# Kernel optimization log

Hardware: AMD Instinct MI355X
Metric: run time of the kernel (lower is better)

## Reference

```python
import jax, jax.numpy as jnp
import numpy as np

B, T, C, H = 4, 2048, 1024, 8
D = C // H


def _rope_tables(t, d, base=10000.0):
    inv = 1.0 / (base ** (jnp.arange(0, d, 2, dtype=jnp.float32) / d))
    freqs = jnp.outer(jnp.arange(t, dtype=jnp.float32), inv)  # (T, D/2)
    cos = jnp.concatenate([jnp.cos(freqs)] * 2, axis=-1)  # (T, D)
    sin = jnp.concatenate([jnp.sin(freqs)] * 2, axis=-1)
    return cos, sin


def _apply_rope(x, cos, sin):
    # x: (B,H,T,D); rotate-half RoPE
    d2 = x.shape[-1] // 2
    x1, x2 = x[..., :d2], x[..., d2:]
    rot = jnp.concatenate([-x2, x1], axis=-1)
    return x * cos + rot * sin


def setup_inputs() -> dict:
    key = jax.random.key(0)
    ks = jax.random.split(key, 8)
    x = jax.random.normal(ks[0], (B, T, C), jnp.float32)
    w = lambda k: jax.random.normal(k, (C, C), jnp.float32) * 0.02
    # trigram directions: 8 sign patterns in {-1,+1}^3, L2-normalized (as in get_trigrams + F.normalize)
    signs = np.array([[(1 if (i >> b) & 1 else -1) for b in range(3)] for i in range(8)], np.float32)
    head_dirs = jnp.asarray(signs / np.sqrt(3.0))
    return {
        'x': x,
        'Wq': w(ks[1]), 'Wk': w(ks[2]), 'Wv': w(ks[3]), 'Wo': w(ks[4]),
        'ln_g': jnp.ones((C,), jnp.float32), 'ln_b': jnp.zeros((C,), jnp.float32),
        'head_scales': jax.random.normal(ks[5], (H,), jnp.float32) * 0.1,
        'head_dirs': head_dirs,
    }


def reference(x, Wq, Wk, Wv, Wo, ln_g, ln_b, head_scales, head_dirs):
    b, t, c = x.shape
    h = head_dirs.shape[0]
    d = c // h
    scale = 1.0 / jnp.sqrt(jnp.asarray(d, x.dtype))
    # pre-LN
    mu = jnp.mean(x, axis=-1, keepdims=True)
    var = jnp.mean((x - mu) ** 2, axis=-1, keepdims=True)
    xn = (x - mu) * jax.lax.rsqrt(var + 1e-5) * ln_g + ln_b
    q = (xn @ Wq.T).reshape(b, t, h, d).transpose(0, 2, 1, 3)  # (B,H,T,D)
    k = (xn @ Wk.T).reshape(b, t, h, d).transpose(0, 2, 1, 3)
    v = (xn @ Wv.T).reshape(b, t, h, d).transpose(0, 2, 1, 3)
    cos, sin = _rope_tables(t, d)
    q = _apply_rope(q, cos, sin)
    k = _apply_rope(k, cos, sin)
    causal = jnp.tril(jnp.ones((t, t), bool))
    # standard causal SDPA
    scores = jnp.einsum('bhqd,bhkd->bhqk', q, k) * scale
    scores = jnp.where(causal, scores, -jnp.inf)
    attn = jax.nn.softmax(scores, axis=-1)
    out = jnp.einsum('bhqk,bhkd->bhqd', attn, v)
    # trigram geometric bias attention (rank-1 logits from first 3 dims)
    qp = jnp.einsum('bhtd,hd->bht', q[..., :3], head_dirs)
    kp = jnp.einsum('bhtd,hd->bht', k[..., :3], head_dirs)
    geo = qp[..., :, None] * kp[..., None, :]  # (B,H,T,T)
    geo = jnp.where(causal, geo, -jnp.inf)
    geo_attn = jax.nn.softmax(geo, axis=-1)
    geo_out = jnp.einsum('bhqk,bhkd->bhqd', geo_attn, v)
    out = out + head_scales[None, :, None, None] * jax.lax.stop_gradient(geo_out - out)
    out = out.transpose(0, 2, 1, 3).reshape(b, t, c) @ Wo.T
    return x + out
```

## Files before the change

kernel.cpp:

```cpp
#include <hip/hip_runtime.h>
#include <hip/hip_bf16.h>
#include <stdint.h>

#define BB 4
#define TT 2048
#define CC 1024
#define HH 8
#define DD 128

typedef unsigned short u16;
typedef unsigned int u32;
typedef unsigned long long u64;
typedef __attribute__((ext_vector_type(4))) float f32x4;
typedef __attribute__((ext_vector_type(16))) float f32x16;
typedef __attribute__((ext_vector_type(8))) __bf16 bf16x8;

#define SL2C (0.08838834764831845f * 1.442695040888963f)

__device__ __forceinline__ float bf2f(u16 u){ u32 x=((u32)u)<<16; float f; __builtin_memcpy(&f,&x,4); return f; }
__device__ __forceinline__ u16 f2bf(float f){ u32 x; __builtin_memcpy(&x,&f,4); x += 0x7fffu + ((x>>16)&1u); return (u16)(x>>16); }

__device__ __forceinline__ void gload16(const void* g, void* l){
  __builtin_amdgcn_global_load_lds((const __attribute__((address_space(1))) u32*)g,
                                   (__attribute__((address_space(3))) u32*)l, 16, 0, 0);
}
__device__ __forceinline__ f32x4 mfma16(bf16x8 a, bf16x8 b, f32x4 c){
  return __builtin_amdgcn_mfma_f32_16x16x32_bf16(a,b,c,0,0,0);
}
__device__ __forceinline__ f32x16 mfma32(bf16x8 a, bf16x8 b, f32x16 c){
  return __builtin_amdgcn_mfma_f32_32x32x16_bf16(a,b,c,0,0,0);
}
__device__ __forceinline__ u32 cvtpk(float lo, float hi){
  u32 r; asm("v_cvt_pk_bf16_f32 %0, %1, %2" : "=v"(r) : "v"(lo), "v"(hi)); return r;
}
__device__ __forceinline__ void pl32swap(u32& d, u32& s){
  asm volatile("v_permlane32_swap_b32 %0, %1" : "+v"(d), "+v"(s));
}
union FRAG { u32 u[4]; bf16x8 v; };

__global__ void ln_k(const float* __restrict__ x, const float* __restrict__ g,
                     const float* __restrict__ bta, u16* __restrict__ xn){
  int row = blockIdx.x, tid = threadIdx.x;
  const float4 v = ((const float4*)(x + (size_t)row*CC))[tid];
  float s = v.x+v.y+v.z+v.w;
  float ss = v.x*v.x+v.y*v.y+v.z*v.z+v.w*v.w;
  #pragma unroll
  for(int m=1;m<64;m<<=1){ s += __shfl_xor(s,m); ss += __shfl_xor(ss,m); }
  __shared__ float red[8];
  if((tid&63)==0){ red[tid>>6]=s; red[4+(tid>>6)]=ss; }
  __syncthreads();
  float ts = red[0]+red[1]+red[2]+red[3];
  float tss = red[4]+red[5]+red[6]+red[7];
  float mu = ts*(1.0f/CC);
  float rs = rsqrtf(tss*(1.0f/CC) - mu*mu + 1e-5f);
  int c0 = tid*4;
  ushort4 o;
  o.x = f2bf((v.x-mu)*rs*g[c0+0]+bta[c0+0]);
  o.y = f2bf((v.y-mu)*rs*g[c0+1]+bta[c0+1]);
  o.z = f2bf((v.z-mu)*rs*g[c0+2]+bta[c0+2]);
  o.w = f2bf((v.w-mu)*rs*g[c0+3]+bta[c0+3]);
  ((ushort4*)(xn + (size_t)row*CC))[tid] = o;
}

__global__ void prep_k(const float* __restrict__ wq, const float* __restrict__ wk,
                       const float* __restrict__ wv, const float* __restrict__ wo,
                       u16* __restrict__ out, float* __restrict__ cosT, float* __restrict__ sinT){
  if(blockIdx.x < 4096){
    int i = blockIdx.x*256 + threadIdx.x;
    int sel = i>>18;
    const float* src = sel==0?wq: sel==1?wk: sel==2?wv:wo;
    float4 v = ((const float4*)src)[i & 262143];
    ushort4 o; o.x=f2bf(v.x); o.y=f2bf(v.y); o.z=f2bf(v.z); o.w=f2bf(v.w);
    ((ushort4*)out)[i] = o;
  } else {
    int i = (blockIdx.x-4096)*256 + threadIdx.x;
    int t = i>>6, j = i&63;
    float inv = powf(10000.0f, -(float)(2*j)*(1.0f/128.0f));
    float a = (float)t * inv;
    cosT[i] = cosf(a);
    sinT[i] = sinf(a);
  }
}

__global__ void qpkp_k(const u16* __restrict__ Qb, const u16* __restrict__ KF,
                       const float* __restrict__ dirs, float* __restrict__ qp, float* __restrict__ kp){
  const float INV_SL2 = 1.0f/SL2C;
  int idx = blockIdx.x*256 + threadIdx.x;
  int b = idx>>14, rem = idx & 16383;
  int h = rem>>11, t = rem & 2047;
  int bh = b*HH + h;
  float d0 = dirs[h*3], d1 = dirs[h*3+1], d2 = dirs[h*3+2];
  size_t qbase = ((size_t)(b*TT + t))*CC + h*DD;
  qp[idx] = (bf2f(Qb[qbase])*d0 + bf2f(Qb[qbase+1])*d1 + bf2f(Qb[qbase+2])*d2) * INV_SL2;
  size_t kb = ((size_t)(bh*64 + (t>>5))*8)*512 + (size_t)(t&31)*8;
  kp[idx] = bf2f(KF[kb])*d0 + bf2f(KF[kb+1])*d1 + bf2f(KF[kb+2])*d2;
}

template<int MODE>
__global__ __launch_bounds__(256) void gemm_k(const u16* __restrict__ A, const u16* __restrict__ W,
                                              u16* __restrict__ outb, float* __restrict__ outf,
                                              const float* __restrict__ resid,
                                              const float* __restrict__ cosT, const float* __restrict__ sinT){
  __shared__ __align__(16) u16 sbuf[16384];
  u16* As = sbuf;
  u16* Bs = sbuf + 8192;
  const int K = CC;
  int m0 = blockIdx.x*128, n0 = blockIdx.y*128;
  int tid = threadIdx.x, w = tid>>6, l = tid&63;
  int li = l&15, lg = l>>4;
  int wm = w>>1, wn = w&1;
  f32x4 acc[4][4] = {};
  for(int k0=0; k0<K; k0+=64){
    #pragma unroll
    for(int i=0;i<4;i++){
      int L = (w*4+i)*1024 + l*16;
      int row = L>>7;
      int colb = (L&127) ^ ((row&7)<<4);
      gload16(A + ((size_t)(m0+row)*K + k0 + (colb>>1)), (char*)As + (w*4+i)*1024);
      gload16(W + ((size_t)(n0+row)*K + k0 + (colb>>1)), (char*)Bs + (w*4+i)*1024);
    }
    __syncthreads();
    #pragma unroll
    for(int kc=0;kc<2;kc++){
      bf16x8 af[4], bfr[4];
      #pragma unroll
      for(int mi=0;mi<4;mi++){
        int row = wm*64 + mi*16 + li;
        int colb = (kc*64 + lg*16) ^ ((row&7)<<4);
        af[mi] = *(const bf16x8*)((const char*)As + row*128 + colb);
      }
      #pragma unroll
      for(int ni=0;ni<4;ni++){
        int row = wn*64 + ni*16 + li;
        int colb = (kc*64 + lg*16) ^ ((row&7)<<4);
        bfr[ni] = *(const bf16x8*)((const char*)Bs + row*128 + colb);
      }
      #pragma unroll
      for(int mi=0;mi<4;mi++){
        #pragma unroll
        for(int ni=0;ni<4;ni++)
          acc[mi][ni] = mfma16(af[mi], bfr[ni], acc[mi][ni]);
      }
    }
    __syncthreads();
  }

  if(MODE==0 || MODE==5){
    #pragma unroll
    for(int mi=0;mi<4;mi++){
      #pragma unroll
      for(int ni=0;ni<4;ni++){
        int c = wn*64 + ni*16 + li;
        #pragma unroll
        for(int r=0;r<4;r++){
          int rr = wm*64 + mi*16 + lg*4 + r;
          sbuf[rr*128 + (c ^ ((rr&15)<<3))] = f2bf(acc[mi][ni][r]);
        }
      }
    }
    __syncthreads();
    int rowl = tid & 127, half = tid >> 7;
    int grow = m0 + rowl;
    int t = grow & (TT-1);
    int swz = (rowl&15)<<3;
    const float* cbase = cosT + t*64;
    const float* sbase = sinT + t*64;
    #pragma unroll
    for(int g=0; g<16; g++){
      int c0 = half*64 + g*4;
      int j0 = c0 & 63;
      float4 cv = *(const float4*)(cbase + j0);
      float4 sv4 = *(const float4*)(sbase + j0);
      ushort4 se4 = *(const ushort4*)&sbuf[rowl*128 + (c0 ^ swz)];
      ushort4 pa4 = *(const ushort4*)&sbuf[rowl*128 + ((c0^64) ^ swz)];
      float se[4] = {bf2f(se4.x),bf2f(se4.y),bf2f(se4.z),bf2f(se4.w)};
      float pa[4] = {bf2f(pa4.x),bf2f(pa4.y),bf2f(pa4.z),bf2f(pa4.w)};
      float cc4[4] = {cv.x,cv.y,cv.z,cv.w};
      float ss4[4] = {sv4.x,sv4.y,sv4.z,sv4.w};
      ushort4 o; u16* op = (u16*)&o;
      #pragma unroll
      for(int e=0;e<4;e++){
        float v = half ? (se[e]*cc4[e] + pa[e]*ss4[e]) : (se[e]*cc4[e] - pa[e]*ss4[e]);
        if(MODE==0) v *= SL2C;
        op[e] = f2bf(v);
      }
      if(MODE==0){
        *(ushort4*)(outb + (size_t)grow*CC + n0 + c0) = o;
      } else {
        int b = grow>>11;
        int h = n0>>7;
        int bh = b*HH + h;
        int d0 = c0;
        size_t of = (((size_t)(bh*64 + (t>>5))*8) + (d0>>4))*512 + (((d0>>3)&1)*32 + (t&31))*8 + (d0&7);
        *(ushort4*)(outb + of) = o;
      }
    }
    return;
  }

  #pragma unroll
  for(int mi=0;mi<4;mi++){
    #pragma unroll
    for(int ni=0;ni<4;ni++){
      if(MODE==4){
        int row0 = m0 + wm*64 + mi*16 + lg*4;
        int col = n0 + wn*64 + ni*16 + li;
        int t = row0 & 2047, b = row0>>11;
        int h = col>>7, d = col&127;
        int bh = b*HH + h;
        size_t o = (((size_t)(bh*64 + (t>>5))*8) + (d>>5)*2 + ((t>>4)&1))*512
                   + (((t>>3)&1)*32 + (d&31))*8 + (t&7);
        ushort4 pk;
        pk.x = f2bf(acc[mi][ni][0]); pk.y = f2bf(acc[mi][ni][1]);
        pk.z = f2bf(acc[mi][ni][2]); pk.w = f2bf(acc[mi][ni][3]);
        *(ushort4*)(outb + o) = pk;
      } else {
        #pragma unroll
        for(int r=0;r<4;r++){
          int row = m0 + wm*64 + mi*16 + lg*4 + r;
          int col = n0 + wn*64 + ni*16 + li;
          size_t o = (size_t)row*CC + col;
          outf[o] = acc[mi][ni][r] + resid[o];
        }
      }
    }
  }
}

struct SegState { float m1, l1, m2, l2; f32x16 a1[4]; f32x16 a2[4]; };

__device__ __forceinline__ void run_seg(int t, int klo, int khi, int bh, int b, int h,
                                        int l5, int q31,
                                        const u16* __restrict__ Q, const u16* __restrict__ KF,
                                        const u16* __restrict__ VF, const float* __restrict__ qp,
                                        const float* __restrict__ kp, SegState& S){
  const f32x16 zf = {};
  S.m1 = -__builtin_inff(); S.l1 = 0.f; S.m2 = -__builtin_inff(); S.l2 = 0.f;
  #pragma unroll
  for(int dt=0;dt<4;dt++){ S.a1[dt] = zf; S.a2[dt] = zf; }
  if(khi <= klo) return;

  int q0 = t*32, q = q0 + q31;
  bf16x8 qf[8];
  {
    const u16* qbase = Q + ((size_t)(b*TT + q)*CC + h*DD);
    #pragma unroll
    for(int db=0;db<8;db++) qf[db] = *(const bf16x8*)(qbase + db*16 + l5*8);
  }
  const float L2E = 1.442695040888963f;
  bf16x8 qpf;
  {
    float qs = qp[(size_t)bh*TT + q] * L2E;
    u16 qh = f2bf(qs); float qhf = bf2f(qh);
    u16 ql = f2bf(qs - qhf);
    FRAG fq; fq.u[0] = l5? 0u : ((u32)qh | ((u32)qh<<16));
    fq.u[1] = l5? 0u : (u32)ql; fq.u[2]=0; fq.u[3]=0;
    qpf = fq.v;
  }
  const u16* kfp = KF + (size_t)bh*64*4096 + (size_t)klo*4096 + (size_t)(q31 + 32*l5)*8;
  const u16* vfp = VF + (size_t)bh*64*4096 + (size_t)klo*4096 + (size_t)(q31 + 32*l5)*8;
  const float* kpp = kp + (size_t)bh*TT + q31;

  for(int is=klo; is<khi; ++is){
    int ksub = is*32;

    bf16x8 kf0 = *(const bf16x8*)(kfp + 0*512);
    bf16x8 kf1 = *(const bf16x8*)(kfp + 1*512);
    bf16x8 kf2 = *(const bf16x8*)(kfp + 2*512);
    bf16x8 kf3 = *(const bf16x8*)(kfp + 3*512);
    bf16x8 kf4 = *(const bf16x8*)(kfp + 4*512);
    bf16x8 kf5 = *(const bf16x8*)(kfp + 5*512);
    bf16x8 kf6 = *(const bf16x8*)(kfp + 6*512);
    bf16x8 kf7 = *(const bf16x8*)(kfp + 7*512);

    f32x16 s0 = {}, s1a = {};
    __builtin_amdgcn_s_setprio(1);
    s0  = mfma32(kf0, qf[0], s0);  s1a = mfma32(kf1, qf[1], s1a);
    s0  = mfma32(kf2, qf[2], s0);  s1a = mfma32(kf3, qf[3], s1a);
    s0  = mfma32(kf4, qf[4], s0);  s1a = mfma32(kf5, qf[5], s1a);
    s0  = mfma32(kf6, qf[6], s0);  s1a = mfma32(kf7, qf[7], s1a);
    __builtin_amdgcn_s_setprio(0);

    f32x16 gg;
    {
      const f32x16 zf2 = {};
      float kpv = kpp[ksub];
      u16 kh = f2bf(kpv); float khf = bf2f(kh);
      u16 kl = f2bf(kpv - khf);
      FRAG fk; fk.u[0] = l5? 0u : ((u32)kh | ((u32)kl<<16));
      fk.u[1] = l5? 0u : (u32)kh; fk.u[2]=0; fk.u[3]=0;
      gg = mfma32(fk.v, qpf, zf2);
    }

    float sv[16], gv[16];
    #pragma unroll
    for(int rr=0;rr<16;rr++){ sv[rr] = s0[rr]+s1a[rr]; gv[rr] = gg[rr]; }
    if(ksub + 31 > q0){
      #pragma unroll
      for(int rr=0;rr<16;rr++){
        int kg = ksub + (rr&3) + 8*(rr>>2) + 4*l5;
        if(kg > q){ sv[rr] = -__builtin_inff(); gv[rr] = -__builtin_inff(); }
      }
    }

    float mx=-__builtin_inff(), gx=-__builtin_inff();
    #pragma unroll
    for(int rr=0;rr<16;rr++){ mx = fmaxf(mx, sv[rr]); gx = fmaxf(gx, gv[rr]); }
    mx = fmaxf(mx, __shfl_xor(mx,32));
    gx = fmaxf(gx, __shfl_xor(gx,32));
    if(__ballot((mx > S.m1+8.f) | (gx > S.m2+8.f))){
      float mn1 = fmaxf(S.m1,mx), mn2 = fmaxf(S.m2,gx);
      float c1 = exp2f(S.m1-mn1), c2 = exp2f(S.m2-mn2);
      S.l1 *= c1; S.l2 *= c2; S.m1 = mn1; S.m2 = mn2;
      #pragma unroll
      for(int dt=0;dt<4;dt++){ S.a1[dt] *= c1; S.a2[dt] *= c2; }
    }
    float rs1=0.f, rs2=0.f;
    float e1[16], e2[16];
    #pragma unroll
    for(int rr=0;rr<16;rr++){
      e1[rr] = exp2f(sv[rr] - S.m1); rs1 += e1[rr];
      e2[rr] = exp2f(gv[rr] - S.m2); rs2 += e2[rr];
    }
    rs1 += __shfl_xor(rs1,32); rs2 += __shfl_xor(rs2,32);
    S.l1 += rs1; S.l2 += rs2;

    u32 P1[8], P2[8];
    #pragma unroll
    for(int m=0;m<8;m++){ P1[m] = cvtpk(e1[2*m], e1[2*m+1]); P2[m] = cvtpk(e2[2*m], e2[2*m+1]); }
    pl32swap(P1[0],P1[2]); pl32swap(P1[1],P1[3]); pl32swap(P1[4],P1[6]); pl32swap(P1[5],P1[7]);
    pl32swap(P2[0],P2[2]); pl32swap(P2[1],P2[3]); pl32swap(P2[4],P2[6]); pl32swap(P2[5],P2[7]);

    #pragma unroll
    for(int kb2=0;kb2<2;kb2++){
      FRAG f1, f2;
      #pragma unroll
      for(int j2=0;j2<4;j2++){ f1.u[j2] = P1[kb2*4+j2]; f2.u[j2] = P2[kb2*4+j2]; }
      bf16x8 pb1 = f1.v, pb2 = f2.v;
      bf16x8 vf0 = *(const bf16x8*)(vfp + (0+kb2)*512);
      bf16x8 vf1 = *(const bf16x8*)(vfp + (2+kb2)*512);
      bf16x8 vf2 = *(const bf16x8*)(vfp + (4+kb2)*512);
      bf16x8 vf3 = *(const bf16x8*)(vfp + (6+kb2)*512);
      __builtin_amdgcn_s_setprio(1);
      S.a1[0] = mfma32(vf0, pb1, S.a1[0]);  S.a2[0] = mfma32(vf0, pb2, S.a2[0]);
      S.a1[1] = mfma32(vf1, pb1, S.a1[1]);  S.a2[1] = mfma32(vf1, pb2, S.a2[1]);
      S.a1[2] = mfma32(vf2, pb1, S.a1[2]);  S.a2[2] = mfma32(vf2, pb2, S.a2[2]);
      S.a1[3] = mfma32(vf3, pb1, S.a1[3]);  S.a2[3] = mfma32(vf3, pb2, S.a2[3]);
      __builtin_amdgcn_s_setprio(0);
    }
    kfp += 4096; vfp += 4096;
  }
}

__global__ __launch_bounds__(128,2) void attn_k(const u16* __restrict__ Q, const u16* __restrict__ KF,
                                                const u16* __restrict__ VF, const float* __restrict__ qp,
                                                const float* __restrict__ kp, const float* __restrict__ hs,
                                                u16* __restrict__ outp){
  __shared__ __align__(16) float lp1[4*64*16];
  __shared__ __align__(16) float lp2[4*64*16];
  __shared__ float lml[32*4];
  int bid = blockIdx.x;
  int xcd = bid&7, r = bid>>3;
  int bh = xcd*4 + (r&3);
  int p = r>>2;
  int b = bh>>3, h = bh&7;
  int tid = threadIdx.x, w = tid>>6, l = tid&63;
  int l5 = l>>5, q31 = l&31;
  float sh = hs[h];

  SegState S;
  if(w==0){
    run_seg(p, 0, p+1, bh, b, h, l5, q31, Q, KF, VF, qp, kp, S);
    {
      float rl1 = 1.0f/S.l1, rl2 = 1.0f/S.l2;
      int q = p*32 + q31;
      u16* obase = outp + (size_t)(b*TT + q)*CC + h*DD;
      #pragma unroll
      for(int dt=0;dt<4;dt++){
        #pragma unroll
        for(int m=0;m<8;m++){
          float oa1 = S.a1[dt][2*m]*rl1,   oa2 = S.a2[dt][2*m]*rl2;
          float ob1 = S.a1[dt][2*m+1]*rl1, ob2 = S.a2[dt][2*m+1]*rl2;
          float oa = oa1 + sh*(oa2-oa1);
          float ob = ob1 + sh*(ob2-ob1);
          int d = dt*32 + (2*m&3) + 8*(m>>1) + 4*l5;
          *(u32*)(obase + d) = cvtpk(oa, ob);
        }
      }
    }
    run_seg(63-p, 0, 31-p, bh, b, h, l5, q31, Q, KF, VF, qp, kp, S);
    #pragma unroll
    for(int dt=0;dt<4;dt++){
      *(f32x16*)&lp1[(dt*64 + l)*16] = S.a1[dt];
      *(f32x16*)&lp2[(dt*64 + l)*16] = S.a2[dt];
    }
    if(l5==0){
      lml[q31*4+0] = S.m1; lml[q31*4+1] = S.l1;
      lml[q31*4+2] = S.m2; lml[q31*4+3] = S.l2;
    }
    __syncthreads();
  } else {
    run_seg(63-p, 31-p, 64-p, bh, b, h, l5, q31, Q, KF, VF, qp, kp, S);
    __syncthreads();
    float mA1 = lml[q31*4+0], lA1 = lml[q31*4+1];
    float mA2 = lml[q31*4+2], lA2 = lml[q31*4+3];
    float M1 = fmaxf(mA1, S.m1), M2 = fmaxf(mA2, S.m2);
    float wA1 = exp2f(mA1-M1), wB1 = exp2f(S.m1-M1);
    float wA2 = exp2f(mA2-M2), wB2 = exp2f(S.m2-M2);
    float r1 = 1.0f/(wA1*lA1 + wB1*S.l1);
    float r2 = 1.0f/(wA2*lA2 + wB2*S.l2);
    int q = (63-p)*32 + q31;
    u16* obase = outp + (size_t)(b*TT + q)*CC + h*DD;
    #pragma unroll
    for(int dt=0;dt<4;dt++){
      f32x16 pa1 = *(const f32x16*)&lp1[(dt*64 + l)*16];
      f32x16 pa2 = *(const f32x16*)&lp2[(dt*64 + l)*16];
      #pragma unroll
      for(int m=0;m<8;m++){
        float oa1 = (wA1*pa1[2*m]   + wB1*S.a1[dt][2*m])*r1;
        float ob1 = (wA1*pa1[2*m+1] + wB1*S.a1[dt][2*m+1])*r1;
        float oa2 = (wA2*pa2[2*m]   + wB2*S.a2[dt][2*m])*r2;
        float ob2 = (wA2*pa2[2*m+1] + wB2*S.a2[dt][2*m+1])*r2;
        float oa = oa1 + sh*(oa2-oa1);
        float ob = ob1 + sh*(ob2-ob1);
        int d = dt*32 + (2*m&3) + 8*(m>>1) + 4*l5;
        *(u32*)(obase + d) = cvtpk(oa, ob);
      }
    }
  }
}

extern "C" void kernel_launch(void* const* d_in, const int* in_sizes, int n_in,
                              void* d_out, int out_size, void* d_ws, size_t ws_size,
                              hipStream_t stream){
  (void)in_sizes; (void)n_in; (void)out_size; (void)ws_size;
  const float* x   = (const float*)d_in[0];
  const float* Wq  = (const float*)d_in[1];
  const float* Wk  = (const float*)d_in[2];
  const float* Wv  = (const float*)d_in[3];
  const float* Wo  = (const float*)d_in[4];
  const float* lng = (const float*)d_in[5];
  const float* lnb = (const float*)d_in[6];
  const float* hsc = (const float*)d_in[7];
  const float* hdr = (const float*)d_in[8];

  char* ws = (char*)d_ws;
  const size_t MB = 1048576;
  u16* xn   = (u16*)ws;
  u16* wbf  = (u16*)(ws + 16*MB);
  u16* Qb   = (u16*)(ws + 24*MB);
  u16* VF   = (u16*)(ws + 56*MB);
  u16* KF   = (u16*)(ws + 72*MB);
  float* cosT = (float*)(ws + 88*MB);
  float* sinT = cosT + 131072;
  float* qp   = sinT + 131072;
  float* kp   = qp + 65536;

  ln_k<<<8192,256,0,stream>>>(x, lng, lnb, xn);
  prep_k<<<4608,256,0,stream>>>(Wq,Wk,Wv,Wo,wbf,cosT,sinT);
  gemm_k<0><<<dim3(64,8),256,0,stream>>>(xn, wbf,          Qb, nullptr, nullptr, cosT, sinT);
  gemm_k<5><<<dim3(64,8),256,0,stream>>>(xn, wbf+1048576,  KF, nullptr, nullptr, cosT, sinT);
  gemm_k<4><<<dim3(64,8),256,0,stream>>>(xn, wbf+2097152,  VF, nullptr, nullptr, nullptr, nullptr);
  qpkp_k<<<256,256,0,stream>>>(Qb,KF,hdr,qp,kp);
  attn_k<<<1024,128,0,stream>>>(Qb,KF,VF,qp,kp,hsc,xn);
  gemm_k<2><<<dim3(64,8),256,0,stream>>>(xn, wbf+3145728, nullptr, (float*)d_out, x, nullptr, nullptr);
}
```

Baseline: 225.3 us.

## Split fused attention into separate geometric and regular attention kernels

Splits the single attention kernel, which carried two online-softmax accumulators, into two kernels. The first computes the rank-1 geometric attention and writes its bf16 output to a workspace buffer G. The second computes the regular causal attention and blends in G using the head scale. The geometric logits are now plain scalar FMAs instead of an MFMA with a split-bf16 trick. Halving the per-thread accumulator state lowers register pressure so launch bounds can rise from 2 to 3 waves. The cost is a second pass over V, an extra kernel launch, and a write and re-read of the intermediate G buffer.

```diff
diff --git a/kernel.cpp b/kernel.cpp
--- a/kernel.cpp
+++ b/kernel.cpp
@@ -16,6 +16,7 @@
 typedef __attribute__((ext_vector_type(8))) __bf16 bf16x8;
 
 #define SL2C (0.08838834764831845f * 1.442695040888963f)
+#define L2E  1.442695040888963f
 
 __device__ __forceinline__ float bf2f(u16 u){ u32 x=((u32)u)<<16; float f; __builtin_memcpy(&f,&x,4); return f; }
 __device__ __forceinline__ u16 f2bf(float f){ u32 x; __builtin_memcpy(&x,&f,4); x += 0x7fffu + ((x>>16)&1u); return (u16)(x>>16); }
@@ -227,138 +228,238 @@
   }
 }
 
-struct SegState { float m1, l1, m2, l2; f32x16 a1[4]; f32x16 a2[4]; };
-
-__device__ __forceinline__ void run_seg(int t, int klo, int khi, int bh, int b, int h,
+struct GeoState { float m2, l2; f32x16 a2[4]; };
+
+__device__ __forceinline__ void run_geo(int t, int klo, int khi, int bh,
                                         int l5, int q31,
-                                        const u16* __restrict__ Q, const u16* __restrict__ KF,
                                         const u16* __restrict__ VF, const float* __restrict__ qp,
-                                        const float* __restrict__ kp, SegState& S){
+                                        const float* __restrict__ kp, GeoState& S){
   const f32x16 zf = {};
-  S.m1 = -__builtin_inff(); S.l1 = 0.f; S.m2 = -__builtin_inff(); S.l2 = 0.f;
+  S.m2 = -__builtin_inff(); S.l2 = 0.f;
   #pragma unroll
-  for(int dt=0;dt<4;dt++){ S.a1[dt] = zf; S.a2[dt] = zf; }
+  for(int dt=0;dt<4;dt++) S.a2[dt] = zf;
   if(khi <= klo) return;
 
   int q0 = t*32, q = q0 + q31;
-  bf16x8 qf[8];
-  {
-    const u16* qbase = Q + ((size_t)(b*TT + q)*CC + h*DD);
-    #pragma unroll
-    for(int db=0;db<8;db++) qf[db] = *(const bf16x8*)(qbase + db*16 + l5*8);
-  }
-  const float L2E = 1.442695040888963f;
-  bf16x8 qpf;
-  {
-    float qs = qp[(size_t)bh*TT + q] * L2E;
-    u16 qh = f2bf(qs); float qhf = bf2f(qh);
-    u16 ql = f2bf(qs - qhf);
-    FRAG fq; fq.u[0] = l5? 0u : ((u32)qh | ((u32)qh<<16));
-    fq.u[1] = l5? 0u : (u32)ql; fq.u[2]=0; fq.u[3]=0;
-    qpf = fq.v;
-  }
-  const u16* kfp = KF + (size_t)bh*64*4096 + (size_t)klo*4096 + (size_t)(q31 + 32*l5)*8;
+  float qpl = qp[(size_t)bh*TT + q] * L2E;
   const u16* vfp = VF + (size_t)bh*64*4096 + (size_t)klo*4096 + (size_t)(q31 + 32*l5)*8;
-  const float* kpp = kp + (size_t)bh*TT + q31;
+  const float* kpb = kp + (size_t)bh*TT + l5*8;
 
   for(int is=klo; is<khi; ++is){
     int ksub = is*32;
-
-    bf16x8 kf0 = *(const bf16x8*)(kfp + 0*512);
-    bf16x8 kf1 = *(const bf16x8*)(kfp + 1*512);
-    bf16x8 kf2 = *(const bf16x8*)(kfp + 2*512);
-    bf16x8 kf3 = *(const bf16x8*)(kfp + 3*512);
-    bf16x8 kf4 = *(const bf16x8*)(kfp + 4*512);
-    bf16x8 kf5 = *(const bf16x8*)(kfp + 5*512);
-    bf16x8 kf6 = *(const bf16x8*)(kfp + 6*512);
-    bf16x8 kf7 = *(const bf16x8*)(kfp + 7*512);
-
-    f32x16 s0 = {}, s1a = {};
-    __builtin_amdgcn_s_setprio(1);
-    s0  = mfma32(kf0, qf[0], s0);  s1a = mfma32(kf1, qf[1], s1a);
-    s0  = mfma32(kf2, qf[2], s0);  s1a = mfma32(kf3, qf[3], s1a);
-    s0  = mfma32(kf4, qf[4], s0);  s1a = mfma32(kf5, qf[5], s1a);
-    s0  = mfma32(kf6, qf[6], s0);  s1a = mfma32(kf7, qf[7], s1a);
-    __builtin_amdgcn_s_setprio(0);
-
-    f32x16 gg;
-    {
-      const f32x16 zf2 = {};
-      float kpv = kpp[ksub];
-      u16 kh = f2bf(kpv); float khf = bf2f(kh);
-      u16 kl = f2bf(kpv - khf);
-      FRAG fk; fk.u[0] = l5? 0u : ((u32)kh | ((u32)kl<<16));
-      fk.u[1] = l5? 0u : (u32)kh; fk.u[2]=0; fk.u[3]=0;
-      gg = mfma32(fk.v, qpf, zf2);
-    }
-
-    float sv[16], gv[16];
-    #pragma unroll
-    for(int rr=0;rr<16;rr++){ sv[rr] = s0[rr]+s1a[rr]; gv[rr] = gg[rr]; }
+    float lg[16];
+    #pragma unroll
+    for(int kb2=0;kb2<2;kb2++){
+      float4 ka = *(const float4*)(kpb + ksub + kb2*16);
+      float4 kb4 = *(const float4*)(kpb + ksub + kb2*16 + 4);
+      lg[kb2*8+0]=qpl*ka.x;  lg[kb2*8+1]=qpl*ka.y;  lg[kb2*8+2]=qpl*ka.z;  lg[kb2*8+3]=qpl*ka.w;
+      lg[kb2*8+4]=qpl*kb4.x; lg[kb2*8+5]=qpl*kb4.y; lg[kb2*8+6]=qpl*kb4.z; lg[kb2*8+7]=qpl*kb4.w;
+    }
     if(ksub + 31 > q0){
       #pragma unroll
-      for(int rr=0;rr<16;rr++){
-        int kg = ksub + (rr&3) + 8*(rr>>2) + 4*l5;
-        if(kg > q){ sv[rr] = -__builtin_inff(); gv[rr] = -__builtin_inff(); }
-      }
-    }
-
-    float mx=-__builtin_inff(), gx=-__builtin_inff();
-    #pragma unroll
-    for(int rr=0;rr<16;rr++){ mx = fmaxf(mx, sv[rr]); gx = fmaxf(gx, gv[rr]); }
-    mx = fmaxf(mx, __shfl_xor(mx,32));
+      for(int e=0;e<16;e++){
+        int kg = ksub + (e>>3)*16 + l5*8 + (e&7);
+        if(kg > q) lg[e] = -__builtin_inff();
+      }
+    }
+    float gx = -__builtin_inff();
+    #pragma unroll
+    for(int e=0;e<16;e++) gx = fmaxf(gx, lg[e]);
     gx = fmaxf(gx, __shfl_xor(gx,32));
-    if(__ballot((mx > S.m1+8.f) | (gx > S.m2+8.f))){
-      float mn1 = fmaxf(S.m1,mx), mn2 = fmaxf(S.m2,gx);
-      float c1 = exp2f(S.m1-mn1), c2 = exp2f(S.m2-mn2);
-      S.l1 *= c1; S.l2 *= c2; S.m1 = mn1; S.m2 = mn2;
-      #pragma unroll
-      for(int dt=0;dt<4;dt++){ S.a1[dt] *= c1; S.a2[dt] *= c2; }
-    }
-    float rs1=0.f, rs2=0.f;
-    float e1[16], e2[16];
-    #pragma unroll
-    for(int rr=0;rr<16;rr++){
-      e1[rr] = exp2f(sv[rr] - S.m1); rs1 += e1[rr];
-      e2[rr] = exp2f(gv[rr] - S.m2); rs2 += e2[rr];
-    }
-    rs1 += __shfl_xor(rs1,32); rs2 += __shfl_xor(rs2,32);
-    S.l1 += rs1; S.l2 += rs2;
-
-    u32 P1[8], P2[8];
-    #pragma unroll
-    for(int m=0;m<8;m++){ P1[m] = cvtpk(e1[2*m], e1[2*m+1]); P2[m] = cvtpk(e2[2*m], e2[2*m+1]); }
-    pl32swap(P1[0],P1[2]); pl32swap(P1[1],P1[3]); pl32swap(P1[4],P1[6]); pl32swap(P1[5],P1[7]);
-    pl32swap(P2[0],P2[2]); pl32swap(P2[1],P2[3]); pl32swap(P2[4],P2[6]); pl32swap(P2[5],P2[7]);
+    if(__ballot(gx > S.m2+8.f)){
+      float mn2 = fmaxf(S.m2,gx);
+      float c2 = exp2f(S.m2-mn2);
+      S.l2 *= c2; S.m2 = mn2;
+      #pragma unroll
+      for(int dt=0;dt<4;dt++) S.a2[dt] *= c2;
+    }
+    float rs2 = 0.f;
+    #pragma unroll
+    for(int e=0;e<16;e++){ lg[e] = exp2f(lg[e] - S.m2); rs2 += lg[e]; }
+    rs2 += __shfl_xor(rs2,32);
+    S.l2 += rs2;
 
     #pragma unroll
     for(int kb2=0;kb2<2;kb2++){
-      FRAG f1, f2;
-      #pragma unroll
-      for(int j2=0;j2<4;j2++){ f1.u[j2] = P1[kb2*4+j2]; f2.u[j2] = P2[kb2*4+j2]; }
-      bf16x8 pb1 = f1.v, pb2 = f2.v;
+      FRAG f2;
+      #pragma unroll
+      for(int j2=0;j2<4;j2++) f2.u[j2] = cvtpk(lg[kb2*8+2*j2], lg[kb2*8+2*j2+1]);
+      bf16x8 pb2 = f2.v;
       bf16x8 vf0 = *(const bf16x8*)(vfp + (0+kb2)*512);
       bf16x8 vf1 = *(const bf16x8*)(vfp + (2+kb2)*512);
       bf16x8 vf2 = *(const bf16x8*)(vfp + (4+kb2)*512);
       bf16x8 vf3 = *(const bf16x8*)(vfp + (6+kb2)*512);
       __builtin_amdgcn_s_setprio(1);
-      S.a1[0] = mfma32(vf0, pb1, S.a1[0]);  S.a2[0] = mfma32(vf0, pb2, S.a2[0]);
-      S.a1[1] = mfma32(vf1, pb1, S.a1[1]);  S.a2[1] = mfma32(vf1, pb2, S.a2[1]);
-      S.a1[2] = mfma32(vf2, pb1, S.a1[2]);  S.a2[2] = mfma32(vf2, pb2, S.a2[2]);
-      S.a1[3] = mfma32(vf3, pb1, S.a1[3]);  S.a2[3] = mfma32(vf3, pb2, S.a2[3]);
+      S.a2[0] = mfma32(vf0, pb2, S.a2[0]);
+      S.a2[1] = mfma32(vf1, pb2, S.a2[1]);
+      S.a2[2] = mfma32(vf2, pb2, S.a2[2]);
+      S.a2[3] = mfma32(vf3, pb2, S.a2[3]);
       __builtin_amdgcn_s_setprio(0);
     }
+    vfp += 4096;
+  }
+}
+
+__global__ __launch_bounds__(128,3) void attn_geo(const u16* __restrict__ VF, const float* __restrict__ qp,
+                                                  const float* __restrict__ kp, u16* __restrict__ G){
+  __shared__ __align__(16) float lp2[4*64*16];
+  __shared__ float lml[32*2];
+  int bid = blockIdx.x;
+  int xcd = bid&7, r = bid>>3;
+  int bh = xcd*4 + (r&3);
+  int p = r>>2;
+  int b = bh>>3, h = bh&7;
+  int tid = threadIdx.x, w = tid>>6, l = tid&63;
+  int l5 = l>>5, q31 = l&31;
+
+  GeoState S;
+  if(w==0){
+    run_geo(p, 0, p+1, bh, l5, q31, VF, qp, kp, S);
+    {
+      float rl2 = 1.0f/S.l2;
+      int q = p*32 + q31;
+      u16* gb = G + (size_t)(b*TT + q)*CC + h*DD;
+      #pragma unroll
+      for(int dt=0;dt<4;dt++){
+        #pragma unroll
+        for(int m=0;m<8;m++){
+          int d = dt*32 + (2*m&3) + 8*(m>>1) + 4*l5;
+          *(u32*)(gb + d) = cvtpk(S.a2[dt][2*m]*rl2, S.a2[dt][2*m+1]*rl2);
+        }
+      }
+    }
+    run_geo(63-p, 0, 31-p, bh, l5, q31, VF, qp, kp, S);
+    #pragma unroll
+    for(int dt=0;dt<4;dt++) *(f32x16*)&lp2[(dt*64 + l)*16] = S.a2[dt];
+    if(l5==0){ lml[q31*2+0] = S.m2; lml[q31*2+1] = S.l2; }
+    __syncthreads();
+  } else {
+    run_geo(63-p, 31-p, 64-p, bh, l5, q31, VF, qp, kp, S);
+    __syncthreads();
+    float mA = lml[q31*2+0], lA = lml[q31*2+1];
+    float M = fmaxf(mA, S.m2);
+    float wA = exp2f(mA-M), wB = exp2f(S.m2-M);
+    float r2 = 1.0f/(wA*lA + wB*S.l2);
+    int q = (63-p)*32 + q31;
+    u16* gb = G + (size_t)(b*TT + q)*CC + h*DD;
+    #pragma unroll
+    for(int dt=0;dt<4;dt++){
+      f32x16 pa = *(const f32x16*)&lp2[(dt*64 + l)*16];
+      #pragma unroll
+      for(int m=0;m<8;m++){
+        int d = dt*32 + (2*m&3) + 8*(m>>1) + 4*l5;
+        float oa = (wA*pa[2*m]   + wB*S.a2[dt][2*m])*r2;
+        float ob = (wA*pa[2*m+1] + wB*S.a2[dt][2*m+1])*r2;
+        *(u32*)(gb + d) = cvtpk(oa, ob);
+      }
+    }
+  }
+}
+
+struct RegState { float m1, l1; f32x16 a1[4]; };
+
+__device__ __forceinline__ void run_reg(int t, int klo, int khi, int bh, int b, int h,
+                                        int l5, int q31,
+                                        const u16* __restrict__ Q, const u16* __restrict__ KF,
+                                        const u16* __restrict__ VF, RegState& S){
+  const f32x16 zf = {};
+  S.m1 = -__builtin_inff(); S.l1 = 0.f;
+  #pragma unroll
+  for(int dt=0;dt<4;dt++) S.a1[dt] = zf;
+  if(khi <= klo) return;
+
+  int q0 = t*32, q = q0 + q31;
+  bf16x8 qf[8];
+  {
+    const u16* qbase = Q + ((size_t)(b*TT + q)*CC + h*DD);
+    #pragma unroll
+    for(int db=0;db<8;db++) qf[db] = *(const bf16x8*)(qbase + db*16 + l5*8);
+  }
+  const u16* kfp = KF + (size_t)bh*64*4096 + (size_t)klo*4096 + (size_t)(q31 + 32*l5)*8;
+  const u16* vfp = VF + (size_t)bh*64*4096 + (size_t)klo*4096 + (size_t)(q31 + 32*l5)*8;
+
+  for(int is=klo; is<khi; ++is){
+    int ksub = is*32;
+
+    f32x16 s0 = {}, s1a = {};
+    {
+      bf16x8 k0 = *(const bf16x8*)(kfp + 0*512);
+      bf16x8 k1 = *(const bf16x8*)(kfp + 1*512);
+      bf16x8 k2 = *(const bf16x8*)(kfp + 2*512);
+      bf16x8 k3 = *(const bf16x8*)(kfp + 3*512);
+      __builtin_amdgcn_s_setprio(1);
+      s0  = mfma32(k0, qf[0], s0);  s1a = mfma32(k1, qf[1], s1a);
+      s0  = mfma32(k2, qf[2], s0);  s1a = mfma32(k3, qf[3], s1a);
+      __builtin_amdgcn_s_setprio(0);
+      k0 = *(const bf16x8*)(kfp + 4*512);
+      k1 = *(const bf16x8*)(kfp + 5*512);
+      k2 = *(const bf16x8*)(kfp + 6*512);
+      k3 = *(const bf16x8*)(kfp + 7*512);
+      __builtin_amdgcn_s_setprio(1);
+      s0  = mfma32(k0, qf[4], s0);  s1a = mfma32(k1, qf[5], s1a);
+      s0  = mfma32(k2, qf[6], s0);  s1a = mfma32(k3, qf[7], s1a);
+      __builtin_amdgcn_s_setprio(0);
+    }
+
+    float sv[16];
+    #pragma unroll
+    for(int rr=0;rr<16;rr++) sv[rr] = s0[rr]+s1a[rr];
+    if(ksub + 31 > q0){
+      #pragma unroll
+      for(int rr=0;rr<16;rr++){
+        int kg = ksub + (rr&3) + 8*(rr>>2) + 4*l5;
+        if(kg > q) sv[rr] = -__builtin_inff();
+      }
+    }
+
+    float mx=-__builtin_inff();
+    #pragma unroll
+    for(int rr=0;rr<16;rr++) mx = fmaxf(mx, sv[rr]);
+    mx = fmaxf(mx, __shfl_xor(mx,32));
+    if(__ballot(mx > S.m1+8.f)){
+      float mn1 = fmaxf(S.m1,mx);
+      float c1 = exp2f(S.m1-mn1);
+      S.l1 *= c1; S.m1 = mn1;
+      #pragma unroll
+      for(int dt=0;dt<4;dt++) S.a1[dt] *= c1;
+    }
+    float rs1=0.f;
+    #pragma unroll
+    for(int rr=0;rr<16;rr++){ sv[rr] = exp2f(sv[rr] - S.m1); rs1 += sv[rr]; }
+    rs1 += __shfl_xor(rs1,32);
+    S.l1 += rs1;
+
+    u32 P1[8];
+    #pragma unroll
+    for(int m=0;m<8;m++) P1[m] = cvtpk(sv[2*m], sv[2*m+1]);
+    pl32swap(P1[0],P1[2]); pl32swap(P1[1],P1[3]); pl32swap(P1[4],P1[6]); pl32swap(P1[5],P1[7]);
+
+    #pragma unroll
+    for(int kb2=0;kb2<2;kb2++){
+      FRAG f1;
+      #pragma unroll
+      for(int j2=0;j2<4;j2++) f1.u[j2] = P1[kb2*4+j2];
+      bf16x8 pb1 = f1.v;
+      bf16x8 vf0 = *(const bf16x8*)(vfp + (0+kb2)*512);
+      bf16x8 vf1 = *(const bf16x8*)(vfp + (2+kb2)*512);
+      bf16x8 vf2 = *(const bf16x8*)(vfp + (4+kb2)*512);
+      bf16x8 vf3 = *(const bf16x8*)(vfp + (6+kb2)*512);
+      __builtin_amdgcn_s_setprio(1);
+      S.a1[0] = mfma32(vf0, pb1, S.a1[0]);
+      S.a1[1] = mfma32(vf1, pb1, S.a1[1]);
+      S.a1[2] = mfma32(vf2, pb1, S.a1[2]);
+      S.a1[3] = mfma32(vf3, pb1, S.a1[3]);
+      __builtin_amdgcn_s_setprio(0);
+    }
     kfp += 4096; vfp += 4096;
   }
 }
 
-__global__ __launch_bounds__(128,2) void attn_k(const u16* __restrict__ Q, const u16* __restrict__ KF,
-                                                const u16* __restrict__ VF, const float* __restrict__ qp,
-                                                const float* __restrict__ kp, const float* __restrict__ hs,
-                                                u16* __restrict__ outp){
+__global__ __launch_bounds__(128,3) void attn_reg(const u16* __restrict__ Q, const u16* __restrict__ KF,
+                                                  const u16* __restrict__ VF, const u16* __restrict__ G,
+                                                  const float* __restrict__ hs, u16* __restrict__ outp){
   __shared__ __align__(16) float lp1[4*64*16];
-  __shared__ __align__(16) float lp2[4*64*16];
-  __shared__ float lml[32*4];
+  __shared__ float lml[32*2];
   int bid = blockIdx.x;
   int xcd = bid&7, r = bid>>3;
   int bh = xcd*4 + (r&3);
@@ -368,63 +469,52 @@
   int l5 = l>>5, q31 = l&31;
   float sh = hs[h];
 
-  SegState S;
+  RegState S;
   if(w==0){
-    run_seg(p, 0, p+1, bh, b, h, l5, q31, Q, KF, VF, qp, kp, S);
+    run_reg(p, 0, p+1, bh, b, h, l5, q31, Q, KF, VF, S);
     {
-      float rl1 = 1.0f/S.l1, rl2 = 1.0f/S.l2;
+      float rl1 = 1.0f/S.l1;
       int q = p*32 + q31;
-      u16* obase = outp + (size_t)(b*TT + q)*CC + h*DD;
+      const u16* gb = G + (size_t)(b*TT + q)*CC + h*DD;
+      u16* ob = outp + (size_t)(b*TT + q)*CC + h*DD;
       #pragma unroll
       for(int dt=0;dt<4;dt++){
         #pragma unroll
         for(int m=0;m<8;m++){
-          float oa1 = S.a1[dt][2*m]*rl1,   oa2 = S.a2[dt][2*m]*rl2;
-          float ob1 = S.a1[dt][2*m+1]*rl1, ob2 = S.a2[dt][2*m+1]*rl2;
-          float oa = oa1 + sh*(oa2-oa1);
-          float ob = ob1 + sh*(ob2-ob1);
           int d = dt*32 + (2*m&3) + 8*(m>>1) + 4*l5;
-          *(u32*)(obase + d) = cvtpk(oa, ob);
+          u32 gpk = *(const u32*)(gb + d);
+          float g0 = bf2f((u16)gpk), g1 = bf2f((u16)(gpk>>16));
+          float o0 = S.a1[dt][2*m]*rl1, o1v = S.a1[dt][2*m+1]*rl1;
+          *(u32*)(ob + d) = cvtpk(o0 + sh*(g0-o0), o1v + sh*(g1-o1v));
         }
       }
     }
-    run_seg(63-p, 0, 31-p, bh, b, h, l5, q31, Q, KF, VF, qp, kp, S);
+    run_reg(63-p, 0, 31-p, bh, b, h, l5, q31, Q, KF, VF, S);
+    #pragma unroll
+    for(int dt=0;dt<4;dt++) *(f32x16*)&lp1[(dt*64 + l)*16] = S.a1[dt];
+    if(l5==0){ lml[q31*2+0] = S.m1; lml[q31*2+1] = S.l1; }
+    __syncthreads();
+  } else {
+    run_reg(63-p, 31-p, 64-p, bh, b, h, l5, q31, Q, KF, VF, S);
+    __syncthreads();
+    float mA = lml[q31*2+0], lA = lml[q31*2+1];
+    float M = fmaxf(mA, S.m1);
+    float wA = exp2f(mA-M), wB = exp2f(S.m1-M);
+    float r1 = 1.0f/(wA*lA + wB*S.l1);
+    int q = (63-p)*32 + q31;
+    const u16* gb = G + (size_t)(b*TT + q)*CC + h*DD;
+    u16* ob = outp + (size_t)(b*TT + q)*CC + h*DD;
     #pragma unroll
     for(int dt=0;dt<4;dt++){
-      *(f32x16*)&lp1[(dt*64 + l)*16] = S.a1[dt];
-      *(f32x16*)&lp2[(dt*64 + l)*16] = S.a2[dt];
-    }
-    if(l5==0){
-      lml[q31*4+0] = S.m1; lml[q31*4+1] = S.l1;
-      lml[q31*4+2] = S.m2; lml[q31*4+3] = S.l2;
-    }
-    __syncthreads();
-  } else {
-    run_seg(63-p, 31-p, 64-p, bh, b, h, l5, q31, Q, KF, VF, qp, kp, S);
-    __syncthreads();
-    float mA1 = lml[q31*4+0], lA1 = lml[q31*4+1];
-    float mA2 = lml[q31*4+2], lA2 = lml[q31*4+3];
-    float M1 = fmaxf(mA1, S.m1), M2 = fmaxf(mA2, S.m2);
-    float wA1 = exp2f(mA1-M1), wB1 = exp2f(S.m1-M1);
-    float wA2 = exp2f(mA2-M2), wB2 = exp2f(S.m2-M2);
-    float r1 = 1.0f/(wA1*lA1 + wB1*S.l1);
-    float r2 = 1.0f/(wA2*lA2 + wB2*S.l2);
-    int q = (63-p)*32 + q31;
-    u16* obase = outp + (size_t)(b*TT + q)*CC + h*DD;
-    #pragma unroll
-    for(int dt=0;dt<4;dt++){
-      f32x16 pa1 = *(const f32x16*)&lp1[(dt*64 + l)*16];
-      f32x16 pa2 = *(const f32x16*)&lp2[(dt*64 + l)*16];
+      f32x16 pa = *(const f32x16*)&lp1[(dt*64 + l)*16];
       #pragma unroll
       for(int m=0;m<8;m++){
-        float oa1 = (wA1*pa1[2*m]   + wB1*S.a1[dt][2*m])*r1;
-        float ob1 = (wA1*pa1[2*m+1] + wB1*S.a1[dt][2*m+1])*r1;
-        float oa2 = (wA2*pa2[2*m]   + wB2*S.a2[dt][2*m])*r2;
-        float ob2 = (wA2*pa2[2*m+1] + wB2*S.a2[dt][2*m+1])*r2;
-        float oa = oa1 + sh*(oa2-oa1);
-        float ob = ob1 + sh*(ob2-ob1);
         int d = dt*32 + (2*m&3) + 8*(m>>1) + 4*l5;
-        *(u32*)(obase + d) = cvtpk(oa, ob);
+        float o0 = (wA*pa[2*m]   + wB*S.a1[dt][2*m])*r1;
+        float o1v = (wA*pa[2*m+1] + wB*S.a1[dt][2*m+1])*r1;
+        u32 gpk = *(const u32*)(gb + d);
+        float g0 = bf2f((u16)gpk), g1 = bf2f((u16)(gpk>>16));
+        *(u32*)(ob + d) = cvtpk(o0 + sh*(g0-o0), o1v + sh*(g1-o1v));
       }
     }
   }
@@ -449,6 +539,7 @@
   u16* xn   = (u16*)ws;
   u16* wbf  = (u16*)(ws + 16*MB);
   u16* Qb   = (u16*)(ws + 24*MB);
+  u16* G    = (u16*)(ws + 40*MB);
   u16* VF   = (u16*)(ws + 56*MB);
   u16* KF   = (u16*)(ws + 72*MB);
   float* cosT = (float*)(ws + 88*MB);
@@ -462,6 +553,7 @@
   gemm_k<5><<<dim3(64,8),256,0,stream>>>(xn, wbf+1048576,  KF, nullptr, nullptr, cosT, sinT);
   gemm_k<4><<<dim3(64,8),256,0,stream>>>(xn, wbf+2097152,  VF, nullptr, nullptr, nullptr, nullptr);
   qpkp_k<<<256,256,0,stream>>>(Qb,KF,hdr,qp,kp);
-  attn_k<<<1024,128,0,stream>>>(Qb,KF,VF,qp,kp,hsc,xn);
+  attn_geo<<<1024,128,0,stream>>>(VF,qp,kp,G);
+  attn_reg<<<1024,128,0,stream>>>(Qb,KF,VF,G,hsc,xn);
   gemm_k<2><<<dim3(64,8),256,0,stream>>>(xn, wbf+3145728, nullptr, (float*)d_out, x, nullptr, nullptr);
 }
```

After: 252.9 us. 1.12x slower.
